# Kernel tuning notes

Hardware: AMD Instinct MI355X
Metric: run time of the kernel (lower is better)

The kernel has to match this reference:

```python
import jax, jax.numpy as jnp
import numpy as np

EPS = 1e-6
H, HKV, D = 32, 8, 64          # heads, kv heads, head_dim
E, TOP_K, FF = 8, 2, 1024      # experts, top-k, expert intermediate
HID = 2048


def rms_norm(x, w):
    xf = x.astype(jnp.float32)
    var = jnp.mean(xf * xf, axis=-1, keepdims=True)
    return (w * (xf * jax.lax.rsqrt(var + EPS)).astype(x.dtype))


def rotate_half(x):
    x1, x2 = jnp.split(x, 2, axis=-1)
    return jnp.concatenate([-x2, x1], axis=-1)


def apply_rope(q, k, cos, sin):
    # cos/sin: [B,S,rd] -> [B,1,S,rd]
    cos = cos[:, None, :, :]
    sin = sin[:, None, :, :]
    rd = cos.shape[-1]
    q_rot, q_pass = q[..., :rd], q[..., rd:]
    k_rot, k_pass = k[..., :rd], k[..., rd:]
    q_emb = q_rot * cos + rotate_half(q_rot) * sin
    k_emb = k_rot * cos + rotate_half(k_rot) * sin
    return (jnp.concatenate([q_emb, q_pass], -1), jnp.concatenate([k_emb, k_pass], -1))


def attention(x, cos, sin, wq, wk, wv, wo):
    B, S, _ = x.shape
    q = (x @ wq).reshape(B, S, H, D).transpose(0, 2, 1, 3)      # [B,H,S,D]
    k = (x @ wk).reshape(B, S, HKV, D).transpose(0, 2, 1, 3)    # [B,Hk,S,D]
    v = (x @ wv).reshape(B, S, HKV, D).transpose(0, 2, 1, 3)
    q, k = apply_rope(q, k, cos, sin)
    rep = H // HKV
    k = jnp.repeat(k, rep, axis=1)
    v = jnp.repeat(v, rep, axis=1)
    scale = D ** -0.5
    scores = jnp.einsum('bhqd,bhkd->bhqk', q, k) * scale
    causal = jnp.triu(jnp.full((S, S), -jnp.inf, dtype=scores.dtype), k=1)
    scores = scores + causal
    probs = jax.nn.softmax(scores.astype(jnp.float32), axis=-1).astype(q.dtype)
    out = jnp.einsum('bhqk,bhkd->bhqd', probs, v)
    out = out.transpose(0, 2, 1, 3).reshape(B, S, H * D)
    return out @ wo


def moe(x, gate_w, corr_bias, w1, w2, w3):
    B, S, Dm = x.shape
    xf = x.reshape(-1, Dm)                                      # [T, Dm]
    T = xf.shape[0]
    logits = xf @ gate_w                                        # [T, E]
    rw = jax.nn.sigmoid(logits.astype(jnp.float32))
    scores = rw + corr_bias
    _, sel = jax.lax.top_k(scores, TOP_K)                       # [T, k]
    tw = jnp.take_along_axis(rw, sel, axis=-1)
    tw = tw / jnp.sum(tw, axis=-1, keepdims=True)
    # dense [T, E] combine weights (zero for unselected experts)
    cw = jnp.zeros((T, E), dtype=xf.dtype).at[jnp.arange(T)[:, None], sel].set(tw.astype(xf.dtype))
    # run every expert densely, combine with sparse weights (same math as gather/scatter loop)
    h = jax.nn.silu(jnp.einsum('td,edf->etf', xf, w1)) * jnp.einsum('td,edf->etf', xf, w3)
    eo = jnp.einsum('etf,efd->etd', h, w2)                      # [E, T, Dm]
    out = jnp.einsum('etd,te->td', eo, cw)
    return out.reshape(B, S, Dm)


def setup_inputs() -> dict:
    key = jax.random.key(0)
    ks = jax.random.split(key, 16)
    s = 0.02
    return {
        'hidden_states': jax.random.normal(ks[0], (2, 1024, HID), jnp.float32),
        'cos': jax.random.uniform(ks[1], (2, 1024, D), jnp.float32),
        'sin': jax.random.uniform(ks[2], (2, 1024, D), jnp.float32),
        'ln1_w': jnp.ones((HID,), jnp.float32),
        'ln2_w': jnp.ones((HID,), jnp.float32),
        'wq': jax.random.normal(ks[3], (HID, H * D), jnp.float32) * s,
        'wk': jax.random.normal(ks[4], (HID, HKV * D), jnp.float32) * s,
        'wv': jax.random.normal(ks[5], (HID, HKV * D), jnp.float32) * s,
        'wo': jax.random.normal(ks[6], (H * D, HID), jnp.float32) * s,
        'gate_w': jax.random.normal(ks[7], (HID, E), jnp.float32) * s,
        'corr_bias': jnp.zeros((E,), jnp.float32),
        'w1': jax.random.normal(ks[8], (E, HID, FF), jnp.float32) * s,
        'w2': jax.random.normal(ks[9], (E, FF, HID), jnp.float32) * s,
        'w3': jax.random.normal(ks[10], (E, HID, FF), jnp.float32) * s,
    }


def reference(hidden_states, cos, sin, ln1_w, ln2_w, wq, wk, wv, wo, gate_w, corr_bias, w1, w2, w3):
    residual = hidden_states
    h = rms_norm(hidden_states, ln1_w)
    h = attention(h, cos, sin, wq, wk, wv, wo)
    h = residual + h
    residual = h
    h = rms_norm(h, ln2_w)
    h = moe(h, gate_w, corr_bias, w1, w2, w3)
    return residual + h
```

## Files before the change

kernel.cpp:

```cpp
#include <hip/hip_runtime.h>
#include <hip/hip_bf16.h>

#define DEV static __device__ __forceinline__

typedef __attribute__((ext_vector_type(8))) short short8;
typedef __attribute__((ext_vector_type(8))) __bf16 bf16x8;
typedef __attribute__((ext_vector_type(4))) float floatx4;

DEV short f2bf(float f) {
  unsigned u = __builtin_bit_cast(unsigned, f);
  unsigned r = (u + 0x7fffu + ((u >> 16) & 1u)) >> 16;
  return (short)(unsigned short)r;
}
DEV float bf2f(short s) {
  unsigned u = ((unsigned)(unsigned short)s) << 16;
  return __builtin_bit_cast(float, u);
}
DEV floatx4 mfma16(short8 a, short8 b, floatx4 c) {
  return __builtin_amdgcn_mfma_f32_16x16x32_bf16(
      __builtin_bit_cast(bf16x8, a), __builtin_bit_cast(bf16x8, b), c, 0, 0, 0);
}

DEV int sw2(int r) { return (r ^ (r >> 2)) & 3; }

DEV const short* sbase(const short* src, int ld, int row0, int id) {
  int r = id >> 2, cc = id & 3;
  return src + (long)(row0 + r) * ld + ((cc ^ sw2(r)) << 3);
}
DEV const short* sbaseg(const short* src, int ld, const int* rows, int p0, int plim,
                        int id) {
  int r = id >> 2, cc = id & 3;
  int pi = p0 + r;
  if (pi > plim) pi = plim;
  return src + (long)rows[pi] * ld + ((cc ^ sw2(r)) << 3);
}
DEV void sissue(short* ldsbuf, const short* base, int k0, int tid, int slotbase) {
  int wave = tid >> 6;
  __builtin_amdgcn_global_load_lds(
      (const __attribute__((address_space(1))) void*)(base + k0),
      (__attribute__((address_space(3))) void*)(ldsbuf + (slotbase + wave * 64) * 8),
      16, 0, 0);
}
DEV short8 rdfrag(const short* lds, int row, int l4) {
  return *(const short8*)(lds + row * 32 + ((l4 ^ sw2(row)) << 3));
}

__global__ __launch_bounds__(256) void k_gemm_qkv(
    const short* Ah, const short* Al, const short* Bh, const short* Bl,
    short* qbh, short* qbl, short* kbh, short* kbl, short* vbh, short* vbl,
    const float* cs, const float* sn) {
  const int K = 2048;
  __shared__ __align__(16) short AsH[2][4096], AsL[2][4096], BsH[2][2048], BsL[2][2048];
  int tid = threadIdx.x, lane = tid & 63, wave = tid >> 6;
  int l15 = lane & 15, l4 = lane >> 4;
  int m0 = blockIdx.y * 128, n0 = blockIdx.x * 64;

  const short* bAH0 = sbase(Ah, K, m0, tid);
  const short* bAH1 = sbase(Ah, K, m0, tid + 256);
  const short* bAL0 = sbase(Al, K, m0, tid);
  const short* bAL1 = sbase(Al, K, m0, tid + 256);
  const short* bBH0 = sbase(Bh, K, n0, tid);
  const short* bBL0 = sbase(Bl, K, n0, tid);

  auto STAGE = [&](int buf, int k0) {
    sissue(AsH[buf], bAH0, k0, tid, 0);
    sissue(AsH[buf], bAH1, k0, tid, 256);
    sissue(AsL[buf], bAL0, k0, tid, 0);
    sissue(AsL[buf], bAL1, k0, tid, 256);
    sissue(BsH[buf], bBH0, k0, tid, 0);
    sissue(BsL[buf], bBL0, k0, tid, 0);
  };

  floatx4 zero4 = {0.f, 0.f, 0.f, 0.f};
  floatx4 acc[2][4];
#pragma unroll
  for (int i = 0; i < 2; ++i)
#pragma unroll
    for (int j = 0; j < 4; ++j) acc[i][j] = zero4;

  STAGE(0, 0);
  __syncthreads();
  int cur = 0;
  for (int k0 = 0; k0 < K; k0 += 32) {
    if (k0 + 32 < K) STAGE(cur ^ 1, k0 + 32);
    short8 ah[2], al[2], bh2[4], bl2[4];
#pragma unroll
    for (int mi = 0; mi < 2; ++mi) {
      ah[mi] = rdfrag(AsH[cur], wave * 32 + mi * 16 + l15, l4);
      al[mi] = rdfrag(AsL[cur], wave * 32 + mi * 16 + l15, l4);
    }
#pragma unroll
    for (int nt = 0; nt < 4; ++nt) {
      bh2[nt] = rdfrag(BsH[cur], nt * 16 + l15, l4);
      bl2[nt] = rdfrag(BsL[cur], nt * 16 + l15, l4);
    }
#pragma unroll
    for (int mi = 0; mi < 2; ++mi)
#pragma unroll
      for (int nt = 0; nt < 4; ++nt) {
        acc[mi][nt] = mfma16(al[mi], bh2[nt], acc[mi][nt]);
        acc[mi][nt] = mfma16(ah[mi], bl2[nt], acc[mi][nt]);
        acc[mi][nt] = mfma16(ah[mi], bh2[nt], acc[mi][nt]);
      }
    __syncthreads();
    cur ^= 1;
  }

  bool isq = n0 < 2048, isk = (!isq) && n0 < 2560;
  if (isq || isk) {
#pragma unroll
    for (int mi = 0; mi < 2; ++mi)
#pragma unroll
      for (int ntp = 0; ntp < 2; ++ntp)
#pragma unroll
        for (int j = 0; j < 4; ++j) {
          int row = m0 + wave * 32 + mi * 16 + l4 * 4 + j;
          int d = ntp * 16 + l15;
          float x0 = acc[mi][ntp][j], x1 = acc[mi][ntp + 2][j];
          float c0 = cs[row * 64 + d], c1 = cs[row * 64 + d + 32];
          float s0 = sn[row * 64 + d], s1 = sn[row * 64 + d + 32];
          float y0 = x0 * c0 - x1 * s0;
          float y1 = x1 * c1 + x0 * s1;
          if (isq) { y0 *= 0.125f; y1 *= 0.125f; }
          acc[mi][ntp][j] = y0;
          acc[mi][ntp + 2][j] = y1;
        }
  }
  short* Ch; short* Cl; int ldc, coff;
  if (isq)      { Ch = qbh; Cl = qbl; ldc = 2048; coff = n0; }
  else if (isk) { Ch = kbh; Cl = kbl; ldc = 512;  coff = n0 - 2048; }
  else          { Ch = vbh; Cl = vbl; ldc = 512;  coff = n0 - 2560; }
#pragma unroll
  for (int mi = 0; mi < 2; ++mi)
#pragma unroll
    for (int nt = 0; nt < 4; ++nt) {
      int row = m0 + wave * 32 + mi * 16 + l4 * 4;
      int col = coff + nt * 16 + l15;
#pragma unroll
      for (int j = 0; j < 4; ++j) {
        float v = acc[mi][nt][j];
        long ix = (long)(row + j) * ldc + col;
        short hi = f2bf(v);
        Ch[ix] = hi;
        Cl[ix] = f2bf(v - bf2f(hi));
      }
    }
}

__global__ __launch_bounds__(256) void k_gemm_wo(const short* Ah, const short* Al,
                                                 const short* Bh, const short* Bl,
                                                 const float* resid, float* out) {
  const int K = 2048;
  __shared__ __align__(16) short AsH[2][4096], AsL[2][4096], BsH[2][2048], BsL[2][2048];
  int tid = threadIdx.x, lane = tid & 63, wave = tid >> 6;
  int l15 = lane & 15, l4 = lane >> 4;
  int m0 = blockIdx.y * 128, n0 = blockIdx.x * 64;

  const short* bAH0 = sbase(Ah, K, m0, tid);
  const short* bAH1 = sbase(Ah, K, m0, tid + 256);
  const short* bAL0 = sbase(Al, K, m0, tid);
  const short* bAL1 = sbase(Al, K, m0, tid + 256);
  const short* bBH0 = sbase(Bh, K, n0, tid);
  const short* bBL0 = sbase(Bl, K, n0, tid);

  auto STAGE = [&](int buf, int k0) {
    sissue(AsH[buf], bAH0, k0, tid, 0);
    sissue(AsH[buf], bAH1, k0, tid, 256);
    sissue(AsL[buf], bAL0, k0, tid, 0);
    sissue(AsL[buf], bAL1, k0, tid, 256);
    sissue(BsH[buf], bBH0, k0, tid, 0);
    sissue(BsL[buf], bBL0, k0, tid, 0);
  };

  floatx4 zero4 = {0.f, 0.f, 0.f, 0.f};
  floatx4 acc[2][4];
#pragma unroll
  for (int i = 0; i < 2; ++i)
#pragma unroll
    for (int j = 0; j < 4; ++j) acc[i][j] = zero4;

  STAGE(0, 0);
  __syncthreads();
  int cur = 0;
  for (int k0 = 0; k0 < K; k0 += 32) {
    if (k0 + 32 < K) STAGE(cur ^ 1, k0 + 32);
    short8 ah[2], al[2], bh2[4], bl2[4];
#pragma unroll
    for (int mi = 0; mi < 2; ++mi) {
      ah[mi] = rdfrag(AsH[cur], wave * 32 + mi * 16 + l15, l4);
      al[mi] = rdfrag(AsL[cur], wave * 32 + mi * 16 + l15, l4);
    }
#pragma unroll
    for (int nt = 0; nt < 4; ++nt) {
      bh2[nt] = rdfrag(BsH[cur], nt * 16 + l15, l4);
      bl2[nt] = rdfrag(BsL[cur], nt * 16 + l15, l4);
    }
#pragma unroll
    for (int mi = 0; mi < 2; ++mi)
#pragma unroll
      for (int nt = 0; nt < 4; ++nt) {
        acc[mi][nt] = mfma16(al[mi], bh2[nt], acc[mi][nt]);
        acc[mi][nt] = mfma16(ah[mi], bl2[nt], acc[mi][nt]);
        acc[mi][nt] = mfma16(ah[mi], bh2[nt], acc[mi][nt]);
      }
    __syncthreads();
    cur ^= 1;
  }
#pragma unroll
  for (int mi = 0; mi < 2; ++mi)
#pragma unroll
    for (int nt = 0; nt < 4; ++nt) {
      int row = m0 + wave * 32 + mi * 16 + l4 * 4;
      int col = n0 + nt * 16 + l15;
#pragma unroll
      for (int j = 0; j < 4; ++j) {
        long ix = (long)(row + j) * 2048 + col;
        out[ix] = resid[ix] + acc[mi][nt][j];
      }
    }
}

__global__ __launch_bounds__(256) void k_moe_a(const short* X, const short* W1T,
                                               const short* W3T, const int* rows,
                                               const int* cnt, const int* eoff,
                                               short* hh) {
  int e = blockIdx.z;
  int c = cnt[e];
  int mtile = blockIdx.y;
  if (mtile * 128 >= c) return;
  int p0 = eoff[e] + mtile * 128;
  int plim = eoff[e] + c - 1;
  const short* B1 = W1T + (long)e * 1024 * 2048;
  const short* B3 = W3T + (long)e * 1024 * 2048;
  int n0 = blockIdx.x * 64;
  __shared__ __align__(16) short As_[2][4096], B1s[2][2048], B3s[2][2048];
  int tid = threadIdx.x, lane = tid & 63, wave = tid >> 6;
  int l15 = lane & 15, l4 = lane >> 4;

  const short* bA0 = sbaseg(X, 2048, rows, p0, plim, tid);
  const short* bA1 = sbaseg(X, 2048, rows, p0, plim, tid + 256);
  const short* bB1 = sbase(B1, 2048, n0, tid);
  const short* bB3 = sbase(B3, 2048, n0, tid);

  auto STAGE = [&](int buf, int k0) {
    sissue(As_[buf], bA0, k0, tid, 0);
    sissue(As_[buf], bA1, k0, tid, 256);
    sissue(B1s[buf], bB1, k0, tid, 0);
    sissue(B3s[buf], bB3, k0, tid, 0);
  };

  floatx4 zero4 = {0.f, 0.f, 0.f, 0.f};
  floatx4 acc1[2][4], acc3[2][4];
#pragma unroll
  for (int i = 0; i < 2; ++i)
#pragma unroll
    for (int j = 0; j < 4; ++j) { acc1[i][j] = zero4; acc3[i][j] = zero4; }

  STAGE(0, 0);
  __syncthreads();
  int cur = 0;
  for (int k0 = 0; k0 < 2048; k0 += 32) {
    if (k0 + 32 < 2048) STAGE(cur ^ 1, k0 + 32);
    short8 af[2], b1f[4], b3f[4];
#pragma unroll
    for (int mi = 0; mi < 2; ++mi) af[mi] = rdfrag(As_[cur], wave * 32 + mi * 16 + l15, l4);
#pragma unroll
    for (int nt = 0; nt < 4; ++nt) {
      b1f[nt] = rdfrag(B1s[cur], nt * 16 + l15, l4);
      b3f[nt] = rdfrag(B3s[cur], nt * 16 + l15, l4);
    }
#pragma unroll
    for (int mi = 0; mi < 2; ++mi)
#pragma unroll
      for (int nt = 0; nt < 4; ++nt) {
        acc1[mi][nt] = mfma16(af[mi], b1f[nt], acc1[mi][nt]);
        acc3[mi][nt] = mfma16(af[mi], b3f[nt], acc3[mi][nt]);
      }
    __syncthreads();
    cur ^= 1;
  }
#pragma unroll
  for (int mi = 0; mi < 2; ++mi)
#pragma unroll
    for (int nt = 0; nt < 4; ++nt) {
      int col = n0 + nt * 16 + l15;
#pragma unroll
      for (int j = 0; j < 4; ++j) {
        int rl = wave * 32 + mi * 16 + l4 * 4 + j;
        if (mtile * 128 + rl < c) {
          float v1 = acc1[mi][nt][j], v3 = acc3[mi][nt][j];
          float hg = v1 / (1.f + __expf(-v1));
          hh[(long)(p0 + rl) * 1024 + col] = f2bf(hg * v3);
        }
      }
    }
}

__global__ __launch_bounds__(256) void k_moe_b(const short* hh, const short* W2T,
                                               const int* cnt, const int* eoff,
                                               short* mo) {
  int e = blockIdx.z;
  int c = cnt[e];
  int mtile = blockIdx.y;
  if (mtile * 128 >= c) return;
  int p0 = eoff[e] + mtile * 128;
  const short* B = W2T + (long)e * 2048 * 1024;
  int n0 = blockIdx.x * 128;
  __shared__ __align__(16) short As_[2][4096], Bs_[2][4096];
  int tid = threadIdx.x, lane = tid & 63, wave = tid >> 6;
  int l15 = lane & 15, l4 = lane >> 4;
  int wm = wave >> 1, wn = wave & 1;

  const short* bA0 = sbase(hh, 1024, p0, tid);
  const short* bA1 = sbase(hh, 1024, p0, tid + 256);
  const short* bB0 = sbase(B, 1024, n0, tid);
  const short* bB1 = sbase(B, 1024, n0, tid + 256);

  auto STAGE = [&](int buf, int k0) {
    sissue(As_[buf], bA0, k0, tid, 0);
    sissue(As_[buf], bA1, k0, tid, 256);
    sissue(Bs_[buf], bB0, k0, tid, 0);
    sissue(Bs_[buf], bB1, k0, tid, 256);
  };

  floatx4 zero4 = {0.f, 0.f, 0.f, 0.f};
  floatx4 acc[4][4];
#pragma unroll
  for (int i = 0; i < 4; ++i)
#pragma unroll
    for (int j = 0; j < 4; ++j) acc[i][j] = zero4;

  STAGE(0, 0);
  __syncthreads();
  int cur = 0;
  for (int k0 = 0; k0 < 1024; k0 += 32) {
    if (k0 + 32 < 1024) STAGE(cur ^ 1, k0 + 32);
    short8 af[4], bfv[4];
#pragma unroll
    for (int mi = 0; mi < 4; ++mi) af[mi] = rdfrag(As_[cur], wm * 64 + mi * 16 + l15, l4);
#pragma unroll
    for (int nt = 0; nt < 4; ++nt) bfv[nt] = rdfrag(Bs_[cur], wn * 64 + nt * 16 + l15, l4);
#pragma unroll
    for (int mi = 0; mi < 4; ++mi)
#pragma unroll
      for (int nt = 0; nt < 4; ++nt) acc[mi][nt] = mfma16(af[mi], bfv[nt], acc[mi][nt]);
    __syncthreads();
    cur ^= 1;
  }
#pragma unroll
  for (int mi = 0; mi < 4; ++mi)
#pragma unroll
    for (int nt = 0; nt < 4; ++nt) {
      int col = n0 + wn * 64 + nt * 16 + l15;
#pragma unroll
      for (int j = 0; j < 4; ++j) {
        int rl = wm * 64 + mi * 16 + l4 * 4 + j;
        if (mtile * 128 + rl < c) mo[(long)(p0 + rl) * 2048 + col] = f2bf(acc[mi][nt][j]);
      }
    }
}

__global__ __launch_bounds__(256) void k_transv(const short* vbh, const short* vbl,
                                                short* vth, short* vtl) {
  __shared__ __align__(16) short th[64][72], tl[64][72];
  int tt = blockIdx.x;
  int bk = blockIdx.y;
  int b = bk >> 3, kvh = bk & 7;
  int tid = threadIdx.x;
#pragma unroll
  for (int it = 0; it < 2; ++it) {
    int id = it * 256 + tid;
    int r = id >> 3, cc = id & 7;
    long src = (long)(b * 1024 + tt * 64 + r) * 512 + kvh * 64 + cc * 8;
    *(uint4*)(&th[r][cc * 8]) = *(const uint4*)(vbh + src);
    *(uint4*)(&tl[r][cc * 8]) = *(const uint4*)(vbl + src);
  }
  __syncthreads();
#pragma unroll
  for (int it = 0; it < 2; ++it) {
    int id = it * 256 + tid;
    int n = id >> 3, kc = id & 7;
    short8 oh2, ol2;
#pragma unroll
    for (int j = 0; j < 8; ++j) { oh2[j] = th[kc * 8 + j][n]; ol2[j] = tl[kc * 8 + j][n]; }
    long dst = (long)bk * 65536 + (long)n * 1024 + tt * 64 + kc * 8;
    *(short8*)(vth + dst) = oh2;
    *(short8*)(vtl + dst) = ol2;
  }
}

DEV int vsw(int r) { return (r ^ (r >> 3)) & 7; }
DEV short8 avread(const short* buf, int row, int c) {
  return *(const short8*)(buf + row * 64 + (((c ^ vsw(row)) & 7) << 3));
}
DEV int aswz(int r, int c) { return r * 64 + (((c ^ ((r ^ (r >> 3)) & 7)) & 7) << 3); }
DEV void glds(short* ldsslot, const short* src) {
  __builtin_amdgcn_global_load_lds(
      (const __attribute__((address_space(1))) void*)src,
      (__attribute__((address_space(3))) void*)ldsslot, 16, 0, 0);
}

__global__ __launch_bounds__(256) void k_attn3(
    const short* qhp, const short* qlp, const short* khp, const short* klp,
    const short* vth2, const short* vtl2, short* oh, short* ol) {
  int xp = blockIdx.x, bh = blockIdx.y;
  int h = bh & 31, b = bh >> 5, kvh = h >> 2;
  int tid = threadIdx.x, wave = tid >> 6, lane = tid & 63;
  int l15 = lane & 15, l4 = lane >> 4;
  int qtA = 15 - xp, qtB = xp;

  __shared__ __align__(16) short Kh[2][4096], Kl[2][4096], Vh[2][4096], Vl[2][4096];
  __shared__ __align__(16) short Ph[4][1024], Pl[4][1024];

  short8 qh[2][2], ql[2][2];
#pragma unroll
  for (int tt = 0; tt < 2; ++tt) {
    int qrow = (tt ? qtB : qtA) * 64 + wave * 16 + l15;
    long qoff = ((long)(b * 1024 + qrow)) * 2048 + h * 64;
    qh[tt][0] = *(const short8*)(qhp + qoff + l4 * 8);
    qh[tt][1] = *(const short8*)(qhp + qoff + 32 + l4 * 8);
    ql[tt][0] = *(const short8*)(qlp + qoff + l4 * 8);
    ql[tt][1] = *(const short8*)(qlp + qoff + 32 + l4 * 8);
  }

  floatx4 zero4 = {0.f, 0.f, 0.f, 0.f};
  floatx4 acco[2][4];
  float mrun[2][4], lrun[2][4];
#pragma unroll
  for (int tt = 0; tt < 2; ++tt)
#pragma unroll
    for (int j = 0; j < 4; ++j) {
      acco[tt][j] = zero4;
      mrun[tt][j] = -1e30f;
      lrun[tt][j] = 0.f;
    }

  const short* khb = khp + ((long)b * 1024) * 512 + kvh * 64;
  const short* klb = klp + ((long)b * 1024) * 512 + kvh * 64;
  const short* vhb = vth2 + (long)(b * 8 + kvh) * 65536;
  const short* vlb = vtl2 + (long)(b * 8 + kvh) * 65536;

  int r0 = tid >> 3, c0 = tid & 7;
  int r1 = r0 + 32;
  const short* kh0 = khb + (long)r0 * 512 + ((c0 ^ vsw(r0)) << 3);
  const short* kh1 = khb + (long)r1 * 512 + ((c0 ^ vsw(r1)) << 3);
  const short* kl0 = klb + (long)r0 * 512 + ((c0 ^ vsw(r0)) << 3);
  const short* kl1 = klb + (long)r1 * 512 + ((c0 ^ vsw(r1)) << 3);
  const short* vh0 = vhb + (long)r0 * 1024 + ((c0 ^ vsw(r0)) << 3);
  const short* vh1 = vhb + (long)r1 * 1024 + ((c0 ^ vsw(r1)) << 3);
  const short* vl0 = vlb + (long)r0 * 1024 + ((c0 ^ vsw(r0)) << 3);
  const short* vl1 = vlb + (long)r1 * 1024 + ((c0 ^ vsw(r1)) << 3);
  int wslot = wave * 512;

  auto STAGE = [&](int buf, int kt) {
    int ko = kt * 32768;
    int vo = kt * 64;
    glds(&Kh[buf][wslot], kh0 + ko);
    glds(&Kh[buf][2048 + wslot], kh1 + ko);
    glds(&Kl[buf][wslot], kl0 + ko);
    glds(&Kl[buf][2048 + wslot], kl1 + ko);
    glds(&Vh[buf][wslot], vh0 + vo);
    glds(&Vh[buf][2048 + wslot], vh1 + vo);
    glds(&Vl[buf][wslot], vl0 + vo);
    glds(&Vl[buf][2048 + wslot], vl1 + vo);
  };

  STAGE(0, 0);
  int cur = 0;
  for (int kt = 0; kt <= qtA; ++kt) {
    __syncthreads();
    if (kt < qtA) STAGE(cur ^ 1, kt + 1);
#pragma unroll
    for (int tt = 0; tt < 2; ++tt) {
      int qtt = tt ? qtB : qtA;
      if (tt == 1 && kt > qtB) continue;
      floatx4 accs[4] = {zero4, zero4, zero4, zero4};
#pragma unroll
      for (int ks = 0; ks < 2; ++ks) {
        short8 qah = qh[tt][ks];
        short8 qal = ql[tt][ks];
#pragma unroll
        for (int nt = 0; nt < 4; ++nt) {
          int kvr = nt * 16 + l15;
          short8 kfh = avread(Kh[cur], kvr, l4 + 4 * ks);
          short8 kfl = avread(Kl[cur], kvr, l4 + 4 * ks);
          accs[nt] = mfma16(qal, kfh, accs[nt]);
          accs[nt] = mfma16(qah, kfl, accs[nt]);
          accs[nt] = mfma16(qah, kfh, accs[nt]);
        }
      }
      if (kt == qtt) {
#pragma unroll
        for (int nt = 0; nt < 4; ++nt)
#pragma unroll
          for (int j = 0; j < 4; ++j) {
            int kvg = nt * 16 + l15;
            int qg = wave * 16 + l4 * 4 + j;
            if (kvg > qg) accs[nt][j] = -1e30f;
          }
      }
      float pj[4][4];
#pragma unroll
      for (int j = 0; j < 4; ++j) {
        float mx = fmaxf(fmaxf(accs[0][j], accs[1][j]), fmaxf(accs[2][j], accs[3][j]));
        mx = fmaxf(mx, __shfl_xor(mx, 1));
        mx = fmaxf(mx, __shfl_xor(mx, 2));
        mx = fmaxf(mx, __shfl_xor(mx, 4));
        mx = fmaxf(mx, __shfl_xor(mx, 8));
        float mnew = fmaxf(mrun[tt][j], mx);
        float alpha = __expf(mrun[tt][j] - mnew);
        float rs = 0.f;
#pragma unroll
        for (int nt = 0; nt < 4; ++nt) {
          float pv = __expf(accs[nt][j] - mnew);
          pj[nt][j] = pv;
          rs += pv;
        }
        rs += __shfl_xor(rs, 1);
        rs += __shfl_xor(rs, 2);
        rs += __shfl_xor(rs, 4);
        rs += __shfl_xor(rs, 8);
        lrun[tt][j] = lrun[tt][j] * alpha + rs;
        mrun[tt][j] = mnew;
        acco[tt][0][j] *= alpha; acco[tt][1][j] *= alpha;
        acco[tt][2][j] *= alpha; acco[tt][3][j] *= alpha;
      }
      short* P = Ph[wave];
      short* P2 = Pl[wave];
#pragma unroll
      for (int nt = 0; nt < 4; ++nt)
#pragma unroll
        for (int j = 0; j < 4; ++j) {
          int rr = l4 * 4 + j, col = nt * 16 + l15;
          float pv = pj[nt][j];
          short hi = f2bf(pv);
          int ad = aswz(rr, col >> 3) + (col & 7);
          P[ad] = hi;
          P2[ad] = f2bf(pv - bf2f(hi));
        }
      asm volatile("s_waitcnt lgkmcnt(0)" ::: "memory");
      __builtin_amdgcn_sched_barrier(0);
#pragma unroll
      for (int ks = 0; ks < 2; ++ks) {
        short8 pah = *(const short8*)(P + aswz(l15, l4 + 4 * ks));
        short8 pal = *(const short8*)(P2 + aswz(l15, l4 + 4 * ks));
#pragma unroll
        for (int nt = 0; nt < 4; ++nt) {
          int dr = nt * 16 + l15;
          short8 vfh = avread(Vh[cur], dr, l4 + 4 * ks);
          short8 vfl = avread(Vl[cur], dr, l4 + 4 * ks);
          acco[tt][nt] = mfma16(pal, vfh, acco[tt][nt]);
          acco[tt][nt] = mfma16(pah, vfl, acco[tt][nt]);
          acco[tt][nt] = mfma16(pah, vfh, acco[tt][nt]);
        }
      }
    }
    cur ^= 1;
  }
#pragma unroll
  for (int tt = 0; tt < 2; ++tt) {
    int qtt = tt ? qtB : qtA;
#pragma unroll
    for (int j = 0; j < 4; ++j) {
      float invl = 1.f / lrun[tt][j];
      int qg = qtt * 64 + wave * 16 + l4 * 4 + j;
      long ooff = ((long)(b * 1024 + qg)) * 2048 + h * 64;
#pragma unroll
      for (int nt = 0; nt < 4; ++nt) {
        float v = acco[tt][nt][j] * invl;
        short hi = f2bf(v);
        oh[ooff + nt * 16 + l15] = hi;
        ol[ooff + nt * 16 + l15] = f2bf(v - bf2f(hi));
      }
    }
  }
}

DEV void trans_load(const float* src, int N, int n0, int k0, float (*t)[65], int tid) {
  int r = tid >> 2, cq = tid & 3;
  const float* s = src + (long)(k0 + r) * N + n0 + cq * 16;
#pragma unroll
  for (int i = 0; i < 4; ++i) {
    float4 v = *(const float4*)(s + i * 4);
    t[r][cq * 16 + i * 4 + 0] = v.x;
    t[r][cq * 16 + i * 4 + 1] = v.y;
    t[r][cq * 16 + i * 4 + 2] = v.z;
    t[r][cq * 16 + i * 4 + 3] = v.w;
  }
}

DEV void trans_tile1(const float* src, short* dst, int N, int K, int n0, int k0,
                     float (*t)[65]) {
  int tid = threadIdx.x;
  trans_load(src, N, n0, k0, t, tid);
  __syncthreads();
  int n = tid >> 2, kc = tid & 3;
#pragma unroll
  for (int ii = 0; ii < 2; ++ii) {
    short8 o;
#pragma unroll
    for (int j = 0; j < 8; ++j) o[j] = f2bf(t[kc * 16 + ii * 8 + j][n]);
    *(short8*)(dst + (long)(n0 + n) * K + k0 + kc * 16 + ii * 8) = o;
  }
}

DEV void trans_tile2(const float* src, short* dh, short* dl, int N, int K, int n0,
                     int k0, float (*t)[65]) {
  int tid = threadIdx.x;
  trans_load(src, N, n0, k0, t, tid);
  __syncthreads();
  int n = tid >> 2, kc = tid & 3;
#pragma unroll
  for (int ii = 0; ii < 2; ++ii) {
    short8 ohv, olv;
#pragma unroll
    for (int j = 0; j < 8; ++j) {
      float v = t[kc * 16 + ii * 8 + j][n];
      short hi = f2bf(v);
      ohv[j] = hi;
      olv[j] = f2bf(v - bf2f(hi));
    }
    *(short8*)(dh + (long)(n0 + n) * K + k0 + kc * 16 + ii * 8) = ohv;
    *(short8*)(dl + (long)(n0 + n) * K + k0 + kc * 16 + ii * 8) = olv;
  }
}

__global__ __launch_bounds__(256) void k_trans_attn(
    const float* wq, const float* wk, const float* wv, const float* wo,
    short* qkvTh, short* qkvTl, short* woTh, short* woTl) {
  __shared__ float t[64][65];
  int x = blockIdx.x, kt = blockIdx.y;
  const float* src; short* dh; short* dl; int N, n0;
  if (x < 32)      { src = wq; dh = qkvTh; dl = qkvTl; N = 2048; n0 = x * 64; }
  else if (x < 40) { src = wk; dh = qkvTh + 2048L * 2048; dl = qkvTl + 2048L * 2048;
                     N = 512; n0 = (x - 32) * 64; }
  else if (x < 48) { src = wv; dh = qkvTh + 2560L * 2048; dl = qkvTl + 2560L * 2048;
                     N = 512; n0 = (x - 40) * 64; }
  else             { src = wo; dh = woTh; dl = woTl; N = 2048; n0 = (x - 48) * 64; }
  trans_tile2(src, dh, dl, N, 2048, n0, kt * 64, t);
}

__global__ __launch_bounds__(256) void k_trans_moe13(const float* w1, const float* w3,
                                                     short* w1T, short* w3T) {
  __shared__ float t[64][65];
  int x = blockIdx.x, kt = blockIdx.y;
  const float* src; short* dst; int n0;
  if (x < 128) { int e = x >> 4; src = w1 + (long)e * 2048 * 1024;
                 dst = w1T + (long)e * 1024 * 2048; n0 = (x & 15) * 64; }
  else         { int i = x - 128, e = i >> 4; src = w3 + (long)e * 2048 * 1024;
                 dst = w3T + (long)e * 1024 * 2048; n0 = (i & 15) * 64; }
  trans_tile1(src, dst, 1024, 2048, n0, kt * 64, t);
}

__global__ __launch_bounds__(256) void k_trans_w2(const float* w2, short* w2T) {
  __shared__ float t[64][65];
  int e = blockIdx.x >> 5, ntb = blockIdx.x & 31, kt = blockIdx.y;
  trans_tile1(w2 + (long)e * 1024 * 2048, w2T + (long)e * 2048 * 1024,
              2048, 1024, ntb * 64, kt * 64, t);
}

__global__ __launch_bounds__(256) void k_rmsnorm1(const float* x, const float* w,
                                                  short* outh, short* outl) {
  int row = blockIdx.x, tid = threadIdx.x;
  const float* xr = x + (long)row * 2048;
  float4 a = *(const float4*)(xr + tid * 8);
  float4 c = *(const float4*)(xr + tid * 8 + 4);
  float ss = a.x * a.x + a.y * a.y + a.z * a.z + a.w * a.w +
             c.x * c.x + c.y * c.y + c.z * c.z + c.w * c.w;
  ss += __shfl_xor(ss, 1);  ss += __shfl_xor(ss, 2);  ss += __shfl_xor(ss, 4);
  ss += __shfl_xor(ss, 8);  ss += __shfl_xor(ss, 16); ss += __shfl_xor(ss, 32);
  __shared__ float red[4];
  int wave = tid >> 6;
  if ((tid & 63) == 0) red[wave] = ss;
  __syncthreads();
  float tot = red[0] + red[1] + red[2] + red[3];
  float inv = 1.f / sqrtf(tot * (1.f / 2048.f) + 1e-6f);
  float4 w0 = *(const float4*)(w + tid * 8);
  float4 w1 = *(const float4*)(w + tid * 8 + 4);
  float xv[8] = {a.x * w0.x, a.y * w0.y, a.z * w0.z, a.w * w0.w,
                 c.x * w1.x, c.y * w1.y, c.z * w1.z, c.w * w1.w};
  short8 ohv, olv;
#pragma unroll
  for (int j = 0; j < 8; ++j) {
    float v = xv[j] * inv;
    short hi = f2bf(v);
    ohv[j] = hi;
    olv[j] = f2bf(v - bf2f(hi));
  }
  *(short8*)(outh + (long)row * 2048 + tid * 8) = ohv;
  *(short8*)(outl + (long)row * 2048 + tid * 8) = olv;
}

__global__ __launch_bounds__(256) void k_rmsnorm2_gate(const float* x, const float* w,
                                                       const float* gw, const float* cb,
                                                       short* out, int* sel, float* tw,
                                                       int* cnt) {
  int row = blockIdx.x, tid = threadIdx.x;
  const float* xr = x + (long)row * 2048;
  float4 a = *(const float4*)(xr + tid * 8);
  float4 c = *(const float4*)(xr + tid * 8 + 4);
  float ss = a.x * a.x + a.y * a.y + a.z * a.z + a.w * a.w +
             c.x * c.x + c.y * c.y + c.z * c.z + c.w * c.w;
  ss += __shfl_xor(ss, 1);  ss += __shfl_xor(ss, 2);  ss += __shfl_xor(ss, 4);
  ss += __shfl_xor(ss, 8);  ss += __shfl_xor(ss, 16); ss += __shfl_xor(ss, 32);
  __shared__ float red[4];
  int wave = tid >> 6;
  if ((tid & 63) == 0) red[wave] = ss;
  __syncthreads();
  float tot = red[0] + red[1] + red[2] + red[3];
  float inv = 1.f / sqrtf(tot * (1.f / 2048.f) + 1e-6f);
  float4 w0 = *(const float4*)(w + tid * 8);
  float4 w1 = *(const float4*)(w + tid * 8 + 4);
  float xn[8];
  xn[0] = a.x * inv * w0.x; xn[1] = a.y * inv * w0.y; xn[2] = a.z * inv * w0.z;
  xn[3] = a.w * inv * w0.w; xn[4] = c.x * inv * w1.x; xn[5] = c.y * inv * w1.y;
  xn[6] = c.z * inv * w1.z; xn[7] = c.w * inv * w1.w;
  short8 o;
#pragma unroll
  for (int j = 0; j < 8; ++j) o[j] = f2bf(xn[j]);
  *(short8*)(out + (long)row * 2048 + tid * 8) = o;
  float gp[8] = {0.f, 0.f, 0.f, 0.f, 0.f, 0.f, 0.f, 0.f};
#pragma unroll
  for (int j = 0; j < 8; ++j) {
    const float* g = gw + (long)(tid * 8 + j) * 8;
    float4 g0 = *(const float4*)g;
    float4 g1 = *(const float4*)(g + 4);
    gp[0] += xn[j] * g0.x; gp[1] += xn[j] * g0.y; gp[2] += xn[j] * g0.z; gp[3] += xn[j] * g0.w;
    gp[4] += xn[j] * g1.x; gp[5] += xn[j] * g1.y; gp[6] += xn[j] * g1.z; gp[7] += xn[j] * g1.w;
  }
#pragma unroll
  for (int e = 0; e < 8; ++e) {
    gp[e] += __shfl_xor(gp[e], 1);  gp[e] += __shfl_xor(gp[e], 2);
    gp[e] += __shfl_xor(gp[e], 4);  gp[e] += __shfl_xor(gp[e], 8);
    gp[e] += __shfl_xor(gp[e], 16); gp[e] += __shfl_xor(gp[e], 32);
  }
  __shared__ float gred[4][8];
  __shared__ float srw[8], ssc[8];
  if ((tid & 63) == 0) {
#pragma unroll
    for (int e = 0; e < 8; ++e) gred[wave][e] = gp[e];
  }
  __syncthreads();
  if (tid < 8) {
    float lg = gred[0][tid] + gred[1][tid] + gred[2][tid] + gred[3][tid];
    float rw = 1.f / (1.f + expf(-lg));
    srw[tid] = rw;
    ssc[tid] = rw + cb[tid];
  }
  __syncthreads();
  if (tid == 0) {
    int e0 = 0; float b0 = ssc[0];
    for (int e = 1; e < 8; ++e) if (ssc[e] > b0) { b0 = ssc[e]; e0 = e; }
    int e1 = -1; float b1 = -1e30f;
    for (int e = 0; e < 8; ++e) if (e != e0 && ssc[e] > b1) { b1 = ssc[e]; e1 = e; }
    float t0 = srw[e0], t1 = srw[e1], s = t0 + t1;
    sel[row * 2] = e0; sel[row * 2 + 1] = e1;
    tw[row * 2] = t0 / s; tw[row * 2 + 1] = t1 / s;
    atomicAdd(&cnt[e0], 1);
    atomicAdd(&cnt[e1], 1);
  }
}

__global__ void k_scan(const int* cnt, int* eoff) {
  if (threadIdx.x == 0) {
    int s = 0;
    for (int e = 0; e < 8; ++e) { eoff[e] = s; s += cnt[e]; }
  }
}

__global__ __launch_bounds__(256) void k_scatter(const int* sel, const int* eoff,
                                                 int* fill, int* rows, int* pos) {
  int t = blockIdx.x * 256 + threadIdx.x;
  if (t >= 2048) return;
  for (int k = 0; k < 2; ++k) {
    int e = sel[t * 2 + k];
    int p = eoff[e] + atomicAdd(&fill[e], 1);
    rows[p] = t;
    pos[t * 2 + k] = p;
  }
}

__global__ __launch_bounds__(256) void k_combine(float* out, const short* mo,
                                                 const int* pos, const float* tw) {
  int t = blockIdx.x, tid = threadIdx.x;
  int p0 = pos[t * 2], p1 = pos[t * 2 + 1];
  float w0 = tw[t * 2], w1 = tw[t * 2 + 1];
  float* o = out + (long)t * 2048 + tid * 8;
  short8 m0 = *(const short8*)(mo + (long)p0 * 2048 + tid * 8);
  short8 m1 = *(const short8*)(mo + (long)p1 * 2048 + tid * 8);
  float4 a = *(const float4*)o;
  float4 b = *(const float4*)(o + 4);
  a.x += w0 * bf2f(m0[0]) + w1 * bf2f(m1[0]);
  a.y += w0 * bf2f(m0[1]) + w1 * bf2f(m1[1]);
  a.z += w0 * bf2f(m0[2]) + w1 * bf2f(m1[2]);
  a.w += w0 * bf2f(m0[3]) + w1 * bf2f(m1[3]);
  b.x += w0 * bf2f(m0[4]) + w1 * bf2f(m1[4]);
  b.y += w0 * bf2f(m0[5]) + w1 * bf2f(m1[5]);
  b.z += w0 * bf2f(m0[6]) + w1 * bf2f(m1[6]);
  b.w += w0 * bf2f(m0[7]) + w1 * bf2f(m1[7]);
  *(float4*)o = a;
  *(float4*)(o + 4) = b;
}

extern "C" void kernel_launch(void* const* d_in, const int* in_sizes, int n_in,
                              void* d_out, int out_size, void* d_ws, size_t ws_size,
                              hipStream_t stream) {
  const float* x    = (const float*)d_in[0];
  const float* cosb = (const float*)d_in[1];
  const float* sinb = (const float*)d_in[2];
  const float* ln1  = (const float*)d_in[3];
  const float* ln2  = (const float*)d_in[4];
  const float* wq   = (const float*)d_in[5];
  const float* wk   = (const float*)d_in[6];
  const float* wv   = (const float*)d_in[7];
  const float* wo   = (const float*)d_in[8];
  const float* gw   = (const float*)d_in[9];
  const float* cb   = (const float*)d_in[10];
  const float* w1   = (const float*)d_in[11];
  const float* w2   = (const float*)d_in[12];
  const float* w3   = (const float*)d_in[13];
  float* out = (float*)d_out;

  char* p = (char*)d_ws;
  auto take = [&](size_t n) { char* r = p; p += (n + 255) & ~(size_t)255; return r; };
  short* qkvTh = (short*)take(3072L * 2048 * 2);
  short* qkvTl = (short*)take(3072L * 2048 * 2);
  short* woTh  = (short*)take(2048L * 2048 * 2);
  short* woTl  = (short*)take(2048L * 2048 * 2);
  short* w1T   = (short*)take(8L * 1024 * 2048 * 2);
  short* w3T   = (short*)take(8L * 1024 * 2048 * 2);
  short* w2T   = (short*)take(8L * 2048 * 1024 * 2);
  short* hbh   = (short*)take(2048L * 2048 * 2);
  short* hbl   = (short*)take(2048L * 2048 * 2);
  short* qbh   = (short*)take(2048L * 2048 * 2);
  short* qbl   = (short*)take(2048L * 2048 * 2);
  short* kbh   = (short*)take(2048L * 512 * 2);
  short* kbl   = (short*)take(2048L * 512 * 2);
  short* vbh   = (short*)take(2048L * 512 * 2);
  short* vbl   = (short*)take(2048L * 512 * 2);
  short* vth   = (short*)take(16L * 64 * 1024 * 2);
  short* vtl   = (short*)take(16L * 64 * 1024 * 2);
  short* aoh   = (short*)take(2048L * 2048 * 2);
  short* aol   = (short*)take(2048L * 2048 * 2);
  short* h2b   = (short*)take(2048L * 2048 * 2);
  short* hhb   = (short*)take(4224L * 1024 * 2);
  short* mob   = (short*)take(4352L * 2048 * 2);
  int* rti     = (int*)take(64 * sizeof(int));
  int* cnt = rti; int* fill = rti + 8; int* eoff = rti + 16;
  int* sel     = (int*)take(2048L * 2 * 4);
  float* twb   = (float*)take(2048L * 2 * 4);
  int* rowsp   = (int*)take(4352L * 4);
  int* posb    = (int*)take(2048L * 2 * 4);
  (void)ws_size; (void)in_sizes; (void)n_in; (void)out_size;

  dim3 B256(256);
  k_trans_attn<<<dim3(80, 32), B256, 0, stream>>>(wq, wk, wv, wo, qkvTh, qkvTl,
                                                  woTh, woTl);
  k_trans_moe13<<<dim3(256, 32), B256, 0, stream>>>(w1, w3, w1T, w3T);
  k_trans_w2<<<dim3(256, 16), B256, 0, stream>>>(w2, w2T);
  hipMemsetAsync(rti, 0, 64, stream);

  k_rmsnorm1<<<dim3(2048), B256, 0, stream>>>(x, ln1, hbh, hbl);
  k_gemm_qkv<<<dim3(48, 16), B256, 0, stream>>>(hbh, hbl, qkvTh, qkvTl, qbh, qbl,
                                                kbh, kbl, vbh, vbl, cosb, sinb);
  k_transv<<<dim3(16, 16), B256, 0, stream>>>(vbh, vbl, vth, vtl);
  k_attn3<<<dim3(8, 64), B256, 0, stream>>>(qbh, qbl, kbh, kbl, vth, vtl, aoh, aol);
  k_gemm_wo<<<dim3(32, 16), B256, 0, stream>>>(aoh, aol, woTh, woTl, x, out);

  k_rmsnorm2_gate<<<dim3(2048), B256, 0, stream>>>(out, ln2, gw, cb, h2b, sel, twb, cnt);
  k_scan<<<dim3(1), dim3(64), 0, stream>>>(cnt, eoff);
  k_scatter<<<dim3(8), B256, 0, stream>>>(sel, eoff, fill, rowsp, posb);
  k_moe_a<<<dim3(16, 16, 8), B256, 0, stream>>>(h2b, w1T, w3T, rowsp, cnt, eoff, hhb);
  k_moe_b<<<dim3(16, 16, 8), B256, 0, stream>>>(hhb, w2T, cnt, eoff, mob);
  k_combine<<<dim3(2048), B256, 0, stream>>>(out, mob, posb, twb);
}
```

Measured before the change: 583.1 us.

## Enlarge GEMM tiles to 128x128 with 2x2 wave layout and block swizzle

```diff
diff --git a/kernel.cpp b/kernel.cpp
--- a/kernel.cpp
+++ b/kernel.cpp
@@ -50,17 +50,23 @@
     short* qbh, short* qbl, short* kbh, short* kbl, short* vbh, short* vbl,
     const float* cs, const float* sn) {
   const int K = 2048;
-  __shared__ __align__(16) short AsH[2][4096], AsL[2][4096], BsH[2][2048], BsL[2][2048];
+  __shared__ __align__(16) short AsH[2][4096], AsL[2][4096], BsH[2][4096], BsL[2][4096];
   int tid = threadIdx.x, lane = tid & 63, wave = tid >> 6;
   int l15 = lane & 15, l4 = lane >> 4;
-  int m0 = blockIdx.y * 128, n0 = blockIdx.x * 64;
+  int wm = wave >> 1, wn = wave & 1;
+  int bid = blockIdx.y * 24 + blockIdx.x;
+  int swz = (bid & 7) * 48 + (bid >> 3);
+  int bx = swz % 24, by = swz / 24;
+  int m0 = by * 128, n0 = bx * 128;
 
   const short* bAH0 = sbase(Ah, K, m0, tid);
   const short* bAH1 = sbase(Ah, K, m0, tid + 256);
   const short* bAL0 = sbase(Al, K, m0, tid);
   const short* bAL1 = sbase(Al, K, m0, tid + 256);
   const short* bBH0 = sbase(Bh, K, n0, tid);
+  const short* bBH1 = sbase(Bh, K, n0, tid + 256);
   const short* bBL0 = sbase(Bl, K, n0, tid);
+  const short* bBL1 = sbase(Bl, K, n0, tid + 256);
 
   auto STAGE = [&](int buf, int k0) {
     sissue(AsH[buf], bAH0, k0, tid, 0);
@@ -68,13 +74,15 @@
     sissue(AsL[buf], bAL0, k0, tid, 0);
     sissue(AsL[buf], bAL1, k0, tid, 256);
     sissue(BsH[buf], bBH0, k0, tid, 0);
+    sissue(BsH[buf], bBH1, k0, tid, 256);
     sissue(BsL[buf], bBL0, k0, tid, 0);
+    sissue(BsL[buf], bBL1, k0, tid, 256);
   };
 
   floatx4 zero4 = {0.f, 0.f, 0.f, 0.f};
-  floatx4 acc[2][4];
-#pragma unroll
-  for (int i = 0; i < 2; ++i)
+  floatx4 acc[4][4];
+#pragma unroll
+  for (int i = 0; i < 4; ++i)
 #pragma unroll
     for (int j = 0; j < 4; ++j) acc[i][j] = zero4;
 
@@ -83,19 +91,19 @@
   int cur = 0;
   for (int k0 = 0; k0 < K; k0 += 32) {
     if (k0 + 32 < K) STAGE(cur ^ 1, k0 + 32);
-    short8 ah[2], al[2], bh2[4], bl2[4];
-#pragma unroll
-    for (int mi = 0; mi < 2; ++mi) {
-      ah[mi] = rdfrag(AsH[cur], wave * 32 + mi * 16 + l15, l4);
-      al[mi] = rdfrag(AsL[cur], wave * 32 + mi * 16 + l15, l4);
+    short8 ah[4], al[4], bh2[4], bl2[4];
+#pragma unroll
+    for (int mi = 0; mi < 4; ++mi) {
+      ah[mi] = rdfrag(AsH[cur], wm * 64 + mi * 16 + l15, l4);
+      al[mi] = rdfrag(AsL[cur], wm * 64 + mi * 16 + l15, l4);
     }
 #pragma unroll
     for (int nt = 0; nt < 4; ++nt) {
-      bh2[nt] = rdfrag(BsH[cur], nt * 16 + l15, l4);
-      bl2[nt] = rdfrag(BsL[cur], nt * 16 + l15, l4);
-    }
-#pragma unroll
-    for (int mi = 0; mi < 2; ++mi)
+      bh2[nt] = rdfrag(BsH[cur], wn * 64 + nt * 16 + l15, l4);
+      bl2[nt] = rdfrag(BsL[cur], wn * 64 + nt * 16 + l15, l4);
+    }
+#pragma unroll
+    for (int mi = 0; mi < 4; ++mi)
 #pragma unroll
       for (int nt = 0; nt < 4; ++nt) {
         acc[mi][nt] = mfma16(al[mi], bh2[nt], acc[mi][nt]);
@@ -106,15 +114,16 @@
     cur ^= 1;
   }
 
-  bool isq = n0 < 2048, isk = (!isq) && n0 < 2560;
+  int hb = n0 + wn * 64;
+  bool isq = hb < 2048, isk = (!isq) && hb < 2560;
   if (isq || isk) {
 #pragma unroll
-    for (int mi = 0; mi < 2; ++mi)
+    for (int mi = 0; mi < 4; ++mi)
 #pragma unroll
       for (int ntp = 0; ntp < 2; ++ntp)
 #pragma unroll
         for (int j = 0; j < 4; ++j) {
-          int row = m0 + wave * 32 + mi * 16 + l4 * 4 + j;
+          int row = m0 + wm * 64 + mi * 16 + l4 * 4 + j;
           int d = ntp * 16 + l15;
           float x0 = acc[mi][ntp][j], x1 = acc[mi][ntp + 2][j];
           float c0 = cs[row * 64 + d], c1 = cs[row * 64 + d + 32];
@@ -127,14 +136,14 @@
         }
   }
   short* Ch; short* Cl; int ldc, coff;
-  if (isq)      { Ch = qbh; Cl = qbl; ldc = 2048; coff = n0; }
-  else if (isk) { Ch = kbh; Cl = kbl; ldc = 512;  coff = n0 - 2048; }
-  else          { Ch = vbh; Cl = vbl; ldc = 512;  coff = n0 - 2560; }
-#pragma unroll
-  for (int mi = 0; mi < 2; ++mi)
+  if (isq)      { Ch = qbh; Cl = qbl; ldc = 2048; coff = hb; }
+  else if (isk) { Ch = kbh; Cl = kbl; ldc = 512;  coff = hb - 2048; }
+  else          { Ch = vbh; Cl = vbl; ldc = 512;  coff = hb - 2560; }
+#pragma unroll
+  for (int mi = 0; mi < 4; ++mi)
 #pragma unroll
     for (int nt = 0; nt < 4; ++nt) {
-      int row = m0 + wave * 32 + mi * 16 + l4 * 4;
+      int row = m0 + wm * 64 + mi * 16 + l4 * 4;
       int col = coff + nt * 16 + l15;
 #pragma unroll
       for (int j = 0; j < 4; ++j) {
@@ -151,17 +160,23 @@
                                                  const short* Bh, const short* Bl,
                                                  const float* resid, float* out) {
   const int K = 2048;
-  __shared__ __align__(16) short AsH[2][4096], AsL[2][4096], BsH[2][2048], BsL[2][2048];
+  __shared__ __align__(16) short AsH[2][4096], AsL[2][4096], BsH[2][4096], BsL[2][4096];
   int tid = threadIdx.x, lane = tid & 63, wave = tid >> 6;
   int l15 = lane & 15, l4 = lane >> 4;
-  int m0 = blockIdx.y * 128, n0 = blockIdx.x * 64;
+  int wm = wave >> 1, wn = wave & 1;
+  int bid = blockIdx.y * 16 + blockIdx.x;
+  int swz = (bid & 7) * 32 + (bid >> 3);
+  int bx = swz % 16, by = swz / 16;
+  int m0 = by * 128, n0 = bx * 128;
 
   const short* bAH0 = sbase(Ah, K, m0, tid);
   const short* bAH1 = sbase(Ah, K, m0, tid + 256);
   const short* bAL0 = sbase(Al, K, m0, tid);
   const short* bAL1 = sbase(Al, K, m0, tid + 256);
   const short* bBH0 = sbase(Bh, K, n0, tid);
+  const short* bBH1 = sbase(Bh, K, n0, tid + 256);
   const short* bBL0 = sbase(Bl, K, n0, tid);
+  const short* bBL1 = sbase(Bl, K, n0, tid + 256);
 
   auto STAGE = [&](int buf, int k0) {
     sissue(AsH[buf], bAH0, k0, tid, 0);
@@ -169,13 +184,15 @@
     sissue(AsL[buf], bAL0, k0, tid, 0);
     sissue(AsL[buf], bAL1, k0, tid, 256);
     sissue(BsH[buf], bBH0, k0, tid, 0);
+    sissue(BsH[buf], bBH1, k0, tid, 256);
     sissue(BsL[buf], bBL0, k0, tid, 0);
+    sissue(BsL[buf], bBL1, k0, tid, 256);
   };
 
   floatx4 zero4 = {0.f, 0.f, 0.f, 0.f};
-  floatx4 acc[2][4];
-#pragma unroll
-  for (int i = 0; i < 2; ++i)
+  floatx4 acc[4][4];
+#pragma unroll
+  for (int i = 0; i < 4; ++i)
 #pragma unroll
     for (int j = 0; j < 4; ++j) acc[i][j] = zero4;
 
@@ -184,19 +201,19 @@
   int cur = 0;
   for (int k0 = 0; k0 < K; k0 += 32) {
     if (k0 + 32 < K) STAGE(cur ^ 1, k0 + 32);
-    short8 ah[2], al[2], bh2[4], bl2[4];
-#pragma unroll
-    for (int mi = 0; mi < 2; ++mi) {
-      ah[mi] = rdfrag(AsH[cur], wave * 32 + mi * 16 + l15, l4);
-      al[mi] = rdfrag(AsL[cur], wave * 32 + mi * 16 + l15, l4);
+    short8 ah[4], al[4], bh2[4], bl2[4];
+#pragma unroll
+    for (int mi = 0; mi < 4; ++mi) {
+      ah[mi] = rdfrag(AsH[cur], wm * 64 + mi * 16 + l15, l4);
+      al[mi] = rdfrag(AsL[cur], wm * 64 + mi * 16 + l15, l4);
     }
 #pragma unroll
     for (int nt = 0; nt < 4; ++nt) {
-      bh2[nt] = rdfrag(BsH[cur], nt * 16 + l15, l4);
-      bl2[nt] = rdfrag(BsL[cur], nt * 16 + l15, l4);
-    }
-#pragma unroll
-    for (int mi = 0; mi < 2; ++mi)
+      bh2[nt] = rdfrag(BsH[cur], wn * 64 + nt * 16 + l15, l4);
+      bl2[nt] = rdfrag(BsL[cur], wn * 64 + nt * 16 + l15, l4);
+    }
+#pragma unroll
+    for (int mi = 0; mi < 4; ++mi)
 #pragma unroll
       for (int nt = 0; nt < 4; ++nt) {
         acc[mi][nt] = mfma16(al[mi], bh2[nt], acc[mi][nt]);
@@ -207,11 +224,11 @@
     cur ^= 1;
   }
 #pragma unroll
-  for (int mi = 0; mi < 2; ++mi)
+  for (int mi = 0; mi < 4; ++mi)
 #pragma unroll
     for (int nt = 0; nt < 4; ++nt) {
-      int row = m0 + wave * 32 + mi * 16 + l4 * 4;
-      int col = n0 + nt * 16 + l15;
+      int row = m0 + wm * 64 + mi * 16 + l4 * 4;
+      int col = n0 + wn * 64 + nt * 16 + l15;
 #pragma unroll
       for (int j = 0; j < 4; ++j) {
         long ix = (long)(row + j) * 2048 + col;
@@ -232,27 +249,32 @@
   int plim = eoff[e] + c - 1;
   const short* B1 = W1T + (long)e * 1024 * 2048;
   const short* B3 = W3T + (long)e * 1024 * 2048;
-  int n0 = blockIdx.x * 64;
-  __shared__ __align__(16) short As_[2][4096], B1s[2][2048], B3s[2][2048];
+  int n0 = blockIdx.x * 128;
+  __shared__ __align__(16) short As_[2][4096], B1s[2][4096], B3s[2][4096];
   int tid = threadIdx.x, lane = tid & 63, wave = tid >> 6;
   int l15 = lane & 15, l4 = lane >> 4;
+  int wm = wave >> 1, wn = wave & 1;
 
   const short* bA0 = sbaseg(X, 2048, rows, p0, plim, tid);
   const short* bA1 = sbaseg(X, 2048, rows, p0, plim, tid + 256);
-  const short* bB1 = sbase(B1, 2048, n0, tid);
-  const short* bB3 = sbase(B3, 2048, n0, tid);
+  const short* bB1_0 = sbase(B1, 2048, n0, tid);
+  const short* bB1_1 = sbase(B1, 2048, n0, tid + 256);
+  const short* bB3_0 = sbase(B3, 2048, n0, tid);
+  const short* bB3_1 = sbase(B3, 2048, n0, tid + 256);
 
   auto STAGE = [&](int buf, int k0) {
     sissue(As_[buf], bA0, k0, tid, 0);
     sissue(As_[buf], bA1, k0, tid, 256);
-    sissue(B1s[buf], bB1, k0, tid, 0);
-    sissue(B3s[buf], bB3, k0, tid, 0);
+    sissue(B1s[buf], bB1_0, k0, tid, 0);
+    sissue(B1s[buf], bB1_1, k0, tid, 256);
+    sissue(B3s[buf], bB3_0, k0, tid, 0);
+    sissue(B3s[buf], bB3_1, k0, tid, 256);
   };
 
   floatx4 zero4 = {0.f, 0.f, 0.f, 0.f};
-  floatx4 acc1[2][4], acc3[2][4];
-#pragma unroll
-  for (int i = 0; i < 2; ++i)
+  floatx4 acc1[4][4], acc3[4][4];
+#pragma unroll
+  for (int i = 0; i < 4; ++i)
 #pragma unroll
     for (int j = 0; j < 4; ++j) { acc1[i][j] = zero4; acc3[i][j] = zero4; }
 
@@ -261,16 +283,16 @@
   int cur = 0;
   for (int k0 = 0; k0 < 2048; k0 += 32) {
     if (k0 + 32 < 2048) STAGE(cur ^ 1, k0 + 32);
-    short8 af[2], b1f[4], b3f[4];
-#pragma unroll
-    for (int mi = 0; mi < 2; ++mi) af[mi] = rdfrag(As_[cur], wave * 32 + mi * 16 + l15, l4);
+    short8 af[4], b1f[4], b3f[4];
+#pragma unroll
+    for (int mi = 0; mi < 4; ++mi) af[mi] = rdfrag(As_[cur], wm * 64 + mi * 16 + l15, l4);
 #pragma unroll
     for (int nt = 0; nt < 4; ++nt) {
-      b1f[nt] = rdfrag(B1s[cur], nt * 16 + l15, l4);
-      b3f[nt] = rdfrag(B3s[cur], nt * 16 + l15, l4);
-    }
-#pragma unroll
-    for (int mi = 0; mi < 2; ++mi)
+      b1f[nt] = rdfrag(B1s[cur], wn * 64 + nt * 16 + l15, l4);
+      b3f[nt] = rdfrag(B3s[cur], wn * 64 + nt * 16 + l15, l4);
+    }
+#pragma unroll
+    for (int mi = 0; mi < 4; ++mi)
 #pragma unroll
       for (int nt = 0; nt < 4; ++nt) {
         acc1[mi][nt] = mfma16(af[mi], b1f[nt], acc1[mi][nt]);
@@ -280,13 +302,13 @@
     cur ^= 1;
   }
 #pragma unroll
-  for (int mi = 0; mi < 2; ++mi)
+  for (int mi = 0; mi < 4; ++mi)
 #pragma unroll
     for (int nt = 0; nt < 4; ++nt) {
-      int col = n0 + nt * 16 + l15;
+      int col = n0 + wn * 64 + nt * 16 + l15;
 #pragma unroll
       for (int j = 0; j < 4; ++j) {
-        int rl = wave * 32 + mi * 16 + l4 * 4 + j;
+        int rl = wm * 64 + mi * 16 + l4 * 4 + j;
         if (mtile * 128 + rl < c) {
           float v1 = acc1[mi][nt][j], v3 = acc3[mi][nt][j];
           float hg = v1 / (1.f + __expf(-v1));
@@ -861,16 +883,16 @@
   hipMemsetAsync(rti, 0, 64, stream);
 
   k_rmsnorm1<<<dim3(2048), B256, 0, stream>>>(x, ln1, hbh, hbl);
-  k_gemm_qkv<<<dim3(48, 16), B256, 0, stream>>>(hbh, hbl, qkvTh, qkvTl, qbh, qbl,
+  k_gemm_qkv<<<dim3(24, 16), B256, 0, stream>>>(hbh, hbl, qkvTh, qkvTl, qbh, qbl,
                                                 kbh, kbl, vbh, vbl, cosb, sinb);
   k_transv<<<dim3(16, 16), B256, 0, stream>>>(vbh, vbl, vth, vtl);
   k_attn3<<<dim3(8, 64), B256, 0, stream>>>(qbh, qbl, kbh, kbl, vth, vtl, aoh, aol);
-  k_gemm_wo<<<dim3(32, 16), B256, 0, stream>>>(aoh, aol, woTh, woTl, x, out);
+  k_gemm_wo<<<dim3(16, 16), B256, 0, stream>>>(aoh, aol, woTh, woTl, x, out);
 
   k_rmsnorm2_gate<<<dim3(2048), B256, 0, stream>>>(out, ln2, gw, cb, h2b, sel, twb, cnt);
   k_scan<<<dim3(1), dim3(64), 0, stream>>>(cnt, eoff);
   k_scatter<<<dim3(8), B256, 0, stream>>>(sel, eoff, fill, rowsp, posb);
-  k_moe_a<<<dim3(16, 16, 8), B256, 0, stream>>>(h2b, w1T, w3T, rowsp, cnt, eoff, hhb);
+  k_moe_a<<<dim3(8, 16, 8), B256, 0, stream>>>(h2b, w1T, w3T, rowsp, cnt, eoff, hhb);
   k_moe_b<<<dim3(16, 16, 8), B256, 0, stream>>>(hhb, w2T, cnt, eoff, mob);
   k_combine<<<dim3(2048), B256, 0, stream>>>(out, mob, posb, twb);
 }
```

After: 663.6 us. 13.8% more time.
